# Kernel optimization log

Measured on AMD Instinct MI355X. Metric: run time of the kernel, lower is better.

Reference implementation:

```python
import jax, jax.numpy as jnp
import numpy as np

EPS = 1e-05  # matches torch module default eps
B, F = 32768, 1024


def setup_inputs() -> dict:
    key = jax.random.key(0)
    x = jax.random.normal(key, (B, F), dtype=jnp.float32)
    M = jnp.zeros((F,), jnp.float32)  # running mean buffer (_M), _n = 0 at init
    S = jnp.zeros((F,), jnp.float32)  # running M2 buffer (_S)
    return {"x": x, "M": M, "S": S}


def _welford(M, S, x):
    """Sequential Welford update over the batch dim, exactly mirroring push()."""
    def step(carry, xi):
        M, S, n = carry
        n1 = n
        n = n + 1
        nf = n.astype(xi.dtype)
        delta = xi - M
        first = n == 1  # first sample ever: M <- x, S unchanged
        M_new = jnp.where(first, xi, M + delta / nf)
        S_new = jnp.where(first, S, S + delta * delta * (n1.astype(xi.dtype) / nf))
        return (M_new, S_new, n), None

    (M, S, n), _ = jax.lax.scan(step, (M, S, jnp.int32(0)), x)
    return M, S, n


def reference(x, M, S):
    M, S, n = _welford(M, S, x)
    nf = n.astype(x.dtype)
    # var = S / (n - 1) if n > 1 else M**2  (module's .var property)
    var = jnp.where(n > 1, S / (nf - 1.0), jnp.square(M))
    # running stats are requires_grad=False buffers in torch -> constants
    mean = jax.lax.stop_gradient(M)
    std = jax.lax.stop_gradient(jnp.sqrt(var))
    return (x - mean) / (std + EPS)
```

## Files before the change

kernel.cpp:

```cpp
#include <hip/hip_runtime.h>
#include <math.h>

#define NFEAT 1024
#define NROWS 32768
#define EPS 1e-5f

#define NB1 1024
#define RPB1 (NROWS / NB1)
#define NCHUNK 32
#define NB3 2048
#define RPB3 (NROWS / NB3)
#define FG (NFEAT / 4)


__global__ __launch_bounds__(256) void reduce1_kernel(
    const float* __restrict__ x, float4* __restrict__ ps, float4* __restrict__ pq)
{
    const int t = threadIdx.x;
    const size_t base = (size_t)(blockIdx.x * RPB1) * FG + t;
    const float4* xv = (const float4*)x;

    float4 s = make_float4(0.f, 0.f, 0.f, 0.f);
    float4 q = make_float4(0.f, 0.f, 0.f, 0.f);

    #pragma unroll
    for (int r = 0; r < RPB1; r += 4) {
        float4 v0 = xv[base + (size_t)(r + 0) * FG];
        float4 v1 = xv[base + (size_t)(r + 1) * FG];
        float4 v2 = xv[base + (size_t)(r + 2) * FG];
        float4 v3 = xv[base + (size_t)(r + 3) * FG];
        s.x += v0.x + v1.x + v2.x + v3.x;
        s.y += v0.y + v1.y + v2.y + v3.y;
        s.z += v0.z + v1.z + v2.z + v3.z;
        s.w += v0.w + v1.w + v2.w + v3.w;
        q.x = fmaf(v0.x, v0.x, fmaf(v1.x, v1.x, fmaf(v2.x, v2.x, fmaf(v3.x, v3.x, q.x))));
        q.y = fmaf(v0.y, v0.y, fmaf(v1.y, v1.y, fmaf(v2.y, v2.y, fmaf(v3.y, v3.y, q.y))));
        q.z = fmaf(v0.z, v0.z, fmaf(v1.z, v1.z, fmaf(v2.z, v2.z, fmaf(v3.z, v3.z, q.z))));
        q.w = fmaf(v0.w, v0.w, fmaf(v1.w, v1.w, fmaf(v2.w, v2.w, fmaf(v3.w, v3.w, q.w))));
    }
    ps[(size_t)blockIdx.x * FG + t] = s;
    pq[(size_t)blockIdx.x * FG + t] = q;
}

__global__ __launch_bounds__(256) void reduce2_kernel(
    const float4* __restrict__ ps, const float4* __restrict__ pq,
    float* __restrict__ sums, float* __restrict__ sumsq)
{
    const int gid = blockIdx.x * 256 + threadIdx.x;
    const int cg = gid & (FG - 1);
    const int chunk = gid >> 8;
    const int b0 = chunk * (NB1 / NCHUNK);

    float4 s = make_float4(0.f, 0.f, 0.f, 0.f);
    float4 q = make_float4(0.f, 0.f, 0.f, 0.f);
    #pragma unroll 8
    for (int i = 0; i < NB1 / NCHUNK; ++i) {
        float4 a = ps[(size_t)(b0 + i) * FG + cg];
        float4 b = pq[(size_t)(b0 + i) * FG + cg];
        s.x += a.x; s.y += a.y; s.z += a.z; s.w += a.w;
        q.x += b.x; q.y += b.y; q.z += b.z; q.w += b.w;
    }
    const int c = 4 * cg;
    atomicAdd(&sums[c + 0], s.x);  atomicAdd(&sums[c + 1], s.y);
    atomicAdd(&sums[c + 2], s.z);  atomicAdd(&sums[c + 3], s.w);
    atomicAdd(&sumsq[c + 0], q.x); atomicAdd(&sumsq[c + 1], q.y);
    atomicAdd(&sumsq[c + 2], q.z); atomicAdd(&sumsq[c + 3], q.w);
}

__global__ __launch_bounds__(256) void norm_kernel(
    const float* __restrict__ x,
    const float* __restrict__ sums, const float* __restrict__ sumsq,
    float* __restrict__ out)
{
    const int t = threadIdx.x;
    const size_t base = (size_t)(blockIdx.x * RPB3) * FG + t;
    const float4* xv = (const float4*)x;
    float4* ov = (float4*)out;

    float4 s = ((const float4*)sums)[t];
    float4 q = ((const float4*)sumsq)[t];

    const float n = (float)NROWS;
    const float rn = 1.0f / n;
    const float rn1 = 1.0f / (n - 1.0f);

    float4 mean, inv;
    mean.x = s.x * rn; mean.y = s.y * rn; mean.z = s.z * rn; mean.w = s.w * rn;
    inv.x = 1.0f / (sqrtf((q.x - s.x * s.x * rn) * rn1) + EPS);
    inv.y = 1.0f / (sqrtf((q.y - s.y * s.y * rn) * rn1) + EPS);
    inv.z = 1.0f / (sqrtf((q.z - s.z * s.z * rn) * rn1) + EPS);
    inv.w = 1.0f / (sqrtf((q.w - s.w * s.w * rn) * rn1) + EPS);

    #pragma unroll
    for (int r = 0; r < RPB3; r += 4) {
        float4 v0 = xv[base + (size_t)(r + 0) * FG];
        float4 v1 = xv[base + (size_t)(r + 1) * FG];
        float4 v2 = xv[base + (size_t)(r + 2) * FG];
        float4 v3 = xv[base + (size_t)(r + 3) * FG];
        float4 o0, o1, o2, o3;
        o0.x = (v0.x - mean.x) * inv.x; o0.y = (v0.y - mean.y) * inv.y;
        o0.z = (v0.z - mean.z) * inv.z; o0.w = (v0.w - mean.w) * inv.w;
        o1.x = (v1.x - mean.x) * inv.x; o1.y = (v1.y - mean.y) * inv.y;
        o1.z = (v1.z - mean.z) * inv.z; o1.w = (v1.w - mean.w) * inv.w;
        o2.x = (v2.x - mean.x) * inv.x; o2.y = (v2.y - mean.y) * inv.y;
        o2.z = (v2.z - mean.z) * inv.z; o2.w = (v2.w - mean.w) * inv.w;
        o3.x = (v3.x - mean.x) * inv.x; o3.y = (v3.y - mean.y) * inv.y;
        o3.z = (v3.z - mean.z) * inv.z; o3.w = (v3.w - mean.w) * inv.w;
        ov[base + (size_t)(r + 0) * FG] = o0;
        ov[base + (size_t)(r + 1) * FG] = o1;
        ov[base + (size_t)(r + 2) * FG] = o2;
        ov[base + (size_t)(r + 3) * FG] = o3;
    }
}

extern "C" void kernel_launch(void* const* d_in, const int* in_sizes, int n_in,
                              void* d_out, int out_size, void* d_ws, size_t ws_size,
                              hipStream_t stream) {
    const float* x = (const float*)d_in[0];
    float* out = (float*)d_out;

    float* sums  = (float*)d_ws;
    float* sumsq = sums + NFEAT;
    float4* ps = (float4*)(sums + 2 * NFEAT);
    float4* pq = ps + (size_t)NB1 * FG;

    hipMemsetAsync(d_ws, 0, 2 * NFEAT * sizeof(float), stream);

    reduce1_kernel<<<NB1, 256, 0, stream>>>(x, ps, pq);
    reduce2_kernel<<<NCHUNK, 256, 0, stream>>>(ps, pq, sums, sumsq);
    norm_kernel<<<NB3, 256, 0, stream>>>(x, sums, sumsq, out);
}
```

Measured before the change: 266.0 us.

## Replace atomic second-stage reduction with per-feature block reduce and nontemporal stores

The second reduction stage now launches one block per float4 feature group and reduces the 1024 partials with a shared-memory tree, replacing the 32-chunk atomicAdd scheme. It also computes mean and inverse std once per feature there instead of in every norm block. The memset launch goes away. The norm kernel writes its output with nontemporal stores to reduce cache pollution. The trade-off is that reduce2 now reads the partials with strided, uncoalesced access, one float4 per row per thread.

Result: no change. 265.8 us (-0.1%).

```diff
diff --git a/kernel.cpp b/kernel.cpp
--- a/kernel.cpp
+++ b/kernel.cpp
@@ -7,10 +7,12 @@
 
 #define NB1 1024
 #define RPB1 (NROWS / NB1)
-#define NCHUNK 32
+#define FG (NFEAT / 4)
+#define NB2 FG
 #define NB3 2048
 #define RPB3 (NROWS / NB3)
-#define FG (NFEAT / 4)
+
+typedef float f32x4 __attribute__((ext_vector_type(4)));
 
 
 __global__ __launch_bounds__(256) void reduce1_kernel(
@@ -44,72 +46,84 @@
 
 __global__ __launch_bounds__(256) void reduce2_kernel(
     const float4* __restrict__ ps, const float4* __restrict__ pq,
-    float* __restrict__ sums, float* __restrict__ sumsq)
+    float4* __restrict__ mean, float4* __restrict__ inv)
 {
-    const int gid = blockIdx.x * 256 + threadIdx.x;
-    const int cg = gid & (FG - 1);
-    const int chunk = gid >> 8;
-    const int b0 = chunk * (NB1 / NCHUNK);
+    const int t = threadIdx.x;
+    const int cg = blockIdx.x;
 
     float4 s = make_float4(0.f, 0.f, 0.f, 0.f);
     float4 q = make_float4(0.f, 0.f, 0.f, 0.f);
-    #pragma unroll 8
-    for (int i = 0; i < NB1 / NCHUNK; ++i) {
-        float4 a = ps[(size_t)(b0 + i) * FG + cg];
-        float4 b = pq[(size_t)(b0 + i) * FG + cg];
+    #pragma unroll
+    for (int k = 0; k < NB1 / 256; ++k) {
+        float4 a = ps[(size_t)(t + 256 * k) * FG + cg];
+        float4 b = pq[(size_t)(t + 256 * k) * FG + cg];
         s.x += a.x; s.y += a.y; s.z += a.z; s.w += a.w;
         q.x += b.x; q.y += b.y; q.z += b.z; q.w += b.w;
     }
-    const int c = 4 * cg;
-    atomicAdd(&sums[c + 0], s.x);  atomicAdd(&sums[c + 1], s.y);
-    atomicAdd(&sums[c + 2], s.z);  atomicAdd(&sums[c + 3], s.w);
-    atomicAdd(&sumsq[c + 0], q.x); atomicAdd(&sumsq[c + 1], q.y);
-    atomicAdd(&sumsq[c + 2], q.z); atomicAdd(&sumsq[c + 3], q.w);
+
+    __shared__ float4 ls[256];
+    __shared__ float4 lq[256];
+    ls[t] = s; lq[t] = q;
+    __syncthreads();
+    #pragma unroll
+    for (int off = 128; off > 0; off >>= 1) {
+        if (t < off) {
+            float4 a = ls[t + off];
+            ls[t].x += a.x; ls[t].y += a.y; ls[t].z += a.z; ls[t].w += a.w;
+            float4 b = lq[t + off];
+            lq[t].x += b.x; lq[t].y += b.y; lq[t].z += b.z; lq[t].w += b.w;
+        }
+        __syncthreads();
+    }
+
+    if (t == 0) {
+        float4 S = ls[0], Q = lq[0];
+        const float n   = (float)NROWS;
+        const float rn  = 1.0f / n;
+        const float rn1 = 1.0f / (n - 1.0f);
+        float4 m, iv;
+        m.x = S.x * rn; m.y = S.y * rn; m.z = S.z * rn; m.w = S.w * rn;
+        iv.x = 1.0f / (sqrtf((Q.x - S.x * S.x * rn) * rn1) + EPS);
+        iv.y = 1.0f / (sqrtf((Q.y - S.y * S.y * rn) * rn1) + EPS);
+        iv.z = 1.0f / (sqrtf((Q.z - S.z * S.z * rn) * rn1) + EPS);
+        iv.w = 1.0f / (sqrtf((Q.w - S.w * S.w * rn) * rn1) + EPS);
+        mean[cg] = m;
+        inv[cg]  = iv;
+    }
 }
 
 __global__ __launch_bounds__(256) void norm_kernel(
     const float* __restrict__ x,
-    const float* __restrict__ sums, const float* __restrict__ sumsq,
+    const float4* __restrict__ mean, const float4* __restrict__ inv,
     float* __restrict__ out)
 {
     const int t = threadIdx.x;
     const size_t base = (size_t)(blockIdx.x * RPB3) * FG + t;
-    const float4* xv = (const float4*)x;
-    float4* ov = (float4*)out;
+    const f32x4* xv = (const f32x4*)x;
+    f32x4* ov = (f32x4*)out;
 
-    float4 s = ((const float4*)sums)[t];
-    float4 q = ((const float4*)sumsq)[t];
-
-    const float n = (float)NROWS;
-    const float rn = 1.0f / n;
-    const float rn1 = 1.0f / (n - 1.0f);
-
-    float4 mean, inv;
-    mean.x = s.x * rn; mean.y = s.y * rn; mean.z = s.z * rn; mean.w = s.w * rn;
-    inv.x = 1.0f / (sqrtf((q.x - s.x * s.x * rn) * rn1) + EPS);
-    inv.y = 1.0f / (sqrtf((q.y - s.y * s.y * rn) * rn1) + EPS);
-    inv.z = 1.0f / (sqrtf((q.z - s.z * s.z * rn) * rn1) + EPS);
-    inv.w = 1.0f / (sqrtf((q.w - s.w * s.w * rn) * rn1) + EPS);
+    const float4 m  = mean[t];
+    const float4 iv = inv[t];
 
     #pragma unroll
     for (int r = 0; r < RPB3; r += 4) {
-        float4 v0 = xv[base + (size_t)(r + 0) * FG];
-        float4 v1 = xv[base + (size_t)(r + 1) * FG];
-        float4 v2 = xv[base + (size_t)(r + 2) * FG];
-        float4 v3 = xv[base + (size_t)(r + 3) * FG];
-        float4 o0, o1, o2, o3;
-        o0.x = (v0.x - mean.x) * inv.x; o0.y = (v0.y - mean.y) * inv.y;
-        o0.z = (v0.z - mean.z) * inv.z; o0.w = (v0.w - mean.w) * inv.w;
-        o1.x = (v1.x - mean.x) * inv.x; o1.y = (v1.y - mean.y) * inv.y;
-        o1.z = (v1.z - mean.z) * inv.z; o1.w = (v1.w - mean.w) * inv.w;
-        o2.x = (v2.x - mean.x) * inv.x; o2.y = (v2.y - mean.y) * inv.y;
-        o2.z = (v2.z - mean.z) * inv.z; o2.w = (v2.w - mean.w) * inv.w;
-        o3.x = (v3.x - mean.x) * inv.x; o3.y = (v3.y - mean.y) * inv.y;
-        o3.z = (v3.z - mean.z) * inv.z; o3.w = (v3.w - mean.w) * inv.w;
-        ov[base + (size_t)(r + 0) * FG] = o0;
-        ov[base + (size_t)(r + 1) * FG] = o1;
-        ov[base + (size_t)(r + 2) * FG] = o2;
-        ov[base + (size_t)(r + 3) * FG] = o3;
+        f32x4 v0 = xv[base + (size_t)(r + 0) * FG];
+        f32x4 v1 = xv[base + (size_t)(r + 1) * FG];
+        f32x4 v2 = xv[base + (size_t)(r + 2) * FG];
+        f32x4 v3 = xv[base + (size_t)(r + 3) * FG];
+        f32x4 o0, o1, o2, o3;
+        o0.x = (v0.x - m.x) * iv.x; o0.y = (v0.y - m.y) * iv.y;
+        o0.z = (v0.z - m.z) * iv.z; o0.w = (v0.w - m.w) * iv.w;
+        o1.x = (v1.x - m.x) * iv.x; o1.y = (v1.y - m.y) * iv.y;
+        o1.z = (v1.z - m.z) * iv.z; o1.w = (v1.w - m.w) * iv.w;
+        o2.x = (v2.x - m.x) * iv.x; o2.y = (v2.y - m.y) * iv.y;
+        o2.z = (v2.z - m.z) * iv.z; o2.w = (v2.w - m.w) * iv.w;
+        o3.x = (v3.x - m.x) * iv.x; o3.y = (v3.y - m.y) * iv.y;
+        o3.z = (v3.z - m.z) * iv.z; o3.w = (v3.w - m.w) * iv.w;
+        __builtin_nontemporal_store(o0, &ov[base + (size_t)(r + 0) * FG]);
+        __builtin_nontemporal_store(o1, &ov[base + (size_t)(r + 1) * FG]);
+        __builtin_nontemporal_store(o2, &ov[base + (size_t)(r + 2) * FG]);
+        __builtin_nontemporal_store(o3, &ov[base + (size_t)(r + 3) * FG]);
     }
 }
 
@@ -119,14 +133,12 @@
     const float* x = (const float*)d_in[0];
     float* out = (float*)d_out;
 
-    float* sums  = (float*)d_ws;
-    float* sumsq = sums + NFEAT;
-    float4* ps = (float4*)(sums + 2 * NFEAT);
+    float* mean = (float*)d_ws;
+    float* inv  = mean + NFEAT;
+    float4* ps = (float4*)(inv + NFEAT);
     float4* pq = ps + (size_t)NB1 * FG;
 
-    hipMemsetAsync(d_ws, 0, 2 * NFEAT * sizeof(float), stream);
-
     reduce1_kernel<<<NB1, 256, 0, stream>>>(x, ps, pq);
-    reduce2_kernel<<<NCHUNK, 256, 0, stream>>>(ps, pq, sums, sumsq);
-    norm_kernel<<<NB3, 256, 0, stream>>>(x, sums, sumsq, out);
+    reduce2_kernel<<<NB2, 256, 0, stream>>>(ps, pq, (float4*)mean, (float4*)inv);
+    norm_kernel<<<NB3, 256, 0, stream>>>(x, (float4*)mean, (float4*)inv, out);
 }
```
